# Kernel tuning notes

Measured on AMD Instinct MI355X. Metric: run time of the kernel, lower is better.

Reference implementation:

```python
import jax, jax.numpy as jnp
import numpy as np

B, S, D, E, K = 4, 4096, 2048, 64, 8

def setup_inputs() -> dict:
    key = jax.random.key(0)
    k1, k2 = jax.random.split(key, 2)
    x = jax.random.normal(k1, (B, S, D), dtype=jnp.float32)
    # centroid projection params (Dense(features=n_experts))
    W = jax.random.normal(k2, (D, E), dtype=jnp.float32) / np.sqrt(D).astype(np.float32)
    b = jnp.zeros((E,), dtype=jnp.float32)
    return {"x": x, "W": W, "b": b, "k": K}

def reference(x, W, b, k):
    # dense gating projection + sigmoid -> per-token expert scores [B,S,E]
    scores = jax.nn.sigmoid(jnp.einsum('bsd,de->bse', x, W) + b)
    # per-token top-k expert selection (vectorized form of apply_along_axis(top))
    g_i, idx = jax.lax.top_k(scores, k)          # [B,S,k]
    g = g_i / jnp.sum(g_i, axis=-1, keepdims=True)  # renormalize top-k gates
    return g, idx, scores
```

## Files before the change

### kernel.cpp

```cpp
#include <hip/hip_runtime.h>
#include <math.h>
#include <stdint.h>

#define NTOK   16384
#define DDIM   2048
#define NE     64
#define TOPK   8

#define THREADS 512
#define TOKPB   32
#define BK      64
#define NCHUNK  (DDIM / BK)

#define XSLOTS   (TOKPB * (BK / 4))
#define WSLOTS   (BK * (NE / 4))
#define BUFSLOTS (XSLOTS + WSLOTS)
#define NBUF     3

__device__ __forceinline__ void gl_lds16(const void* g, void* l) {
    __builtin_amdgcn_global_load_lds(
        (const __attribute__((address_space(1))) void*)(uintptr_t)g,
        (__attribute__((address_space(3))) void*)(uintptr_t)l,
        16, 0, 0);
}

__global__ __launch_bounds__(THREADS, 4) void gate_kernel(
    const float* __restrict__ x, const float* __restrict__ W,
    const float* __restrict__ b, float* __restrict__ out)
{
    __shared__ float4 smem[NBUF * BUFSLOTS];

    const int tid  = threadIdx.x;
    const int wave = tid >> 6;
    const int ks   = tid >> 5;
    const int p    = tid & 31;
    const int tg   = p >> 3;
    const int eg   = p & 7;
    const int tok0 = blockIdx.x * TOKPB;

    const int st_t  = tid >> 4;
    const int st_kp = tid & 15;
    const float* gx  = x + (size_t)(tok0 + st_t) * DDIM
                         + 4 * (st_kp ^ ((st_t >> 3) & 3));
    const float* gw0 = W + (size_t)st_t        * NE + 4 * (st_kp ^ wave);
    const float* gw1 = W + (size_t)(st_t + 32) * NE + 4 * (st_kp ^ wave);

    auto stage = [&](int c) {
        float4* Bf = &smem[(c % NBUF) * BUFSLOTS];
        const int kc = c * BK;
        gl_lds16(gx + kc,               &Bf[wave * 64]);
        gl_lds16(gw0 + (size_t)kc * NE, &Bf[XSLOTS + wave * 64]);
        gl_lds16(gw1 + (size_t)kc * NE, &Bf[XSLOTS + 512 + wave * 64]);
    };

    float acc[8][8];
#pragma unroll
    for (int i = 0; i < 8; ++i)
#pragma unroll
        for (int j = 0; j < 8; ++j) acc[i][j] = 0.f;

    auto compute = [&](int c) {
        const float4* BX = &smem[(c % NBUF) * BUFSLOTS];
        const float4* BW = BX + XSLOTS;
        float4 wreg[4][2];
#pragma unroll
        for (int kk = 0; kk < 4; ++kk) {
            const int k = ks * 4 + kk;
            wreg[kk][0] = BW[k * 16 + ((eg * 2)     ^ (ks & 7))];
            wreg[kk][1] = BW[k * 16 + ((eg * 2 + 1) ^ (ks & 7))];
        }
#pragma unroll
        for (int i = 0; i < 8; ++i) {
            const float4 xv = BX[(tg * 8 + i) * 16 + (ks ^ tg)];
            const float* xp = (const float*)&xv;
#pragma unroll
            for (int kk = 0; kk < 4; ++kk) {
                const float xs = xp[kk];
                const float* w0 = (const float*)&wreg[kk][0];
                const float* w1 = (const float*)&wreg[kk][1];
#pragma unroll
                for (int m = 0; m < 4; ++m) {
                    acc[i][m]     = fmaf(xs, w0[m], acc[i][m]);
                    acc[i][4 + m] = fmaf(xs, w1[m], acc[i][4 + m]);
                }
            }
        }
    };

    stage(0); stage(1);
#pragma unroll 1
    for (int c = 0; c < NCHUNK - 1; ++c) {
        asm volatile("s_waitcnt vmcnt(3)" ::: "memory");
        __builtin_amdgcn_s_barrier();
        if (c + 2 < NCHUNK) stage(c + 2);
        compute(c);
    }
    asm volatile("s_waitcnt vmcnt(0)" ::: "memory");
    __builtin_amdgcn_s_barrier();
    compute(NCHUNK - 1);
    __syncthreads();

#pragma unroll
    for (int i = 0; i < 8; ++i)
#pragma unroll
        for (int j = 0; j < 8; ++j)
            acc[i][j] += __shfl_xor(acc[i][j], 32);

    float* part = (float*)smem;
    if ((tid & 63) < 32) {
        float* dst = part + wave * 2176 + p * 68;
#pragma unroll
        for (int fq = 0; fq < 16; ++fq) {
            const int i = fq >> 1, h = fq & 1;
            *(float4*)(dst + fq * 4) = make_float4(
                acc[i][h * 4], acc[i][h * 4 + 1],
                acc[i][h * 4 + 2], acc[i][h * 4 + 3]);
        }
    }
    __syncthreads();

    const int t  = tid >> 4;
    const int e4 = tid & 15;
    const int cp = ((t >> 3) << 3) + (e4 >> 1);
    const int cf = ((t & 7) << 1) + (e4 & 1);
    const float4* pf4 = (const float4*)part;
    float sx = 0.f, sy = 0.f, sz = 0.f, sw = 0.f;
#pragma unroll
    for (int w = 0; w < 8; ++w) {
        const float4 v = pf4[w * 544 + cp * 17 + cf];
        sx += v.x; sy += v.y; sz += v.z; sw += v.w;
    }
    __syncthreads();

    const float4 bv = *(const float4*)(b + e4 * 4);
    float4 sg;
    sg.x = 1.f / (1.f + expf(-(sx + bv.x)));
    sg.y = 1.f / (1.f + expf(-(sy + bv.y)));
    sg.z = 1.f / (1.f + expf(-(sz + bv.z)));
    sg.w = 1.f / (1.f + expf(-(sw + bv.w)));

    float* out_g   = out;
    float* out_idx = out + (size_t)NTOK * TOPK;
    float* out_s   = out + (size_t)NTOK * TOPK * 2;

    *(float4*)(out_s + (size_t)(tok0 + t) * NE + e4 * 4) = sg;
    float4* sc4 = (float4*)part;
    sc4[t * 17 + e4] = sg;
    __syncthreads();

    if (tid < 256) {
        const int tt = tid >> 3, lg = tid & 7;
        const float4 a0 = sc4[tt * 17 + lg * 2];
        const float4 a1 = sc4[tt * 17 + lg * 2 + 1];
        float s[8] = {a0.x, a0.y, a0.z, a0.w, a1.x, a1.y, a1.z, a1.w};
        float vsel = 0.f; int esel = 0; float ssum = 0.f;
#pragma unroll
        for (int j = 0; j < TOPK; ++j) {
            float bvv = s[0]; int be = 0;
#pragma unroll
            for (int m = 1; m < 8; ++m)
                if (s[m] > bvv) { bvv = s[m]; be = m; }
            float v = bvv; int ec = lg * 8 + be;
#pragma unroll
            for (int d = 1; d < 8; d <<= 1) {
                const float ov = __shfl_xor(v, d);
                const int   oe = __shfl_xor(ec, d);
                if (ov > v || (ov == v && oe < ec)) { v = ov; ec = oe; }
            }
            ssum += v;
            if (lg == j) { vsel = v; esel = ec; }
            if ((ec >> 3) == lg) {
                const int sl = ec & 7;
#pragma unroll
                for (int m = 0; m < 8; ++m)
                    if (sl == m) s[m] = -1.f;
            }
        }
        const float inv = 1.f / ssum;
        out_g  [(size_t)(tok0 + tt) * TOPK + lg] = vsel * inv;
        out_idx[(size_t)(tok0 + tt) * TOPK + lg] = (float)esel;
    }
}

extern "C" void kernel_launch(void* const* d_in, const int* in_sizes, int n_in,
                              void* d_out, int out_size, void* d_ws, size_t ws_size,
                              hipStream_t stream) {
    const float* x = (const float*)d_in[0];
    const float* W = (const float*)d_in[1];
    const float* b = (const float*)d_in[2];
    float* out = (float*)d_out;
    gate_kernel<<<NTOK / TOKPB, THREADS, 0, stream>>>(x, W, b, out);
}
```

Measured before the change: 221.9 us.

## Halve tokens per block, double-buffer, and remap threads to raise occupancy

Cuts tokens per block from 32 to 16 and gives each thread 8x4 accumulators instead of 8x8. Replaces the triple-buffered vmcnt pipeline with a double buffer guarded by a full barrier. Removes the LDS XOR swizzles and wraps compute in s_setprio, with launch bounds raised to 6 blocks per CU. The aim is higher occupancy and fewer registers. In exchange, W tiles are loaded twice as often per token, and the pipeline is shallower with more blocking syncs.

```diff
diff --git a/kernel.cpp b/kernel.cpp
--- a/kernel.cpp
+++ b/kernel.cpp
@@ -8,14 +8,14 @@
 #define TOPK   8
 
 #define THREADS 512
-#define TOKPB   32
+#define TOKPB   16
 #define BK      64
 #define NCHUNK  (DDIM / BK)
 
 #define XSLOTS   (TOKPB * (BK / 4))
 #define WSLOTS   (BK * (NE / 4))
 #define BUFSLOTS (XSLOTS + WSLOTS)
-#define NBUF     3
+#define SMEMF4   (2 * BUFSLOTS)
 
 __device__ __forceinline__ void gl_lds16(const void* g, void* l) {
     __builtin_amdgcn_global_load_lds(
@@ -24,131 +24,120 @@
         16, 0, 0);
 }
 
-__global__ __launch_bounds__(THREADS, 4) void gate_kernel(
+__global__ __launch_bounds__(THREADS, 6) void gate_kernel(
     const float* __restrict__ x, const float* __restrict__ W,
     const float* __restrict__ b, float* __restrict__ out)
 {
-    __shared__ float4 smem[NBUF * BUFSLOTS];
+    __shared__ float4 smem[SMEMF4];
 
     const int tid  = threadIdx.x;
     const int wave = tid >> 6;
+    const int lane = tid & 63;
     const int ks   = tid >> 5;
-    const int p    = tid & 31;
-    const int tg   = p >> 3;
-    const int eg   = p & 7;
+    const int tg   = (tid >> 4) & 1;
+    const int eg   = tid & 15;
     const int tok0 = blockIdx.x * TOKPB;
 
-    const int st_t  = tid >> 4;
-    const int st_kp = tid & 15;
-    const float* gx  = x + (size_t)(tok0 + st_t) * DDIM
-                         + 4 * (st_kp ^ ((st_t >> 3) & 3));
-    const float* gw0 = W + (size_t)st_t        * NE + 4 * (st_kp ^ wave);
-    const float* gw1 = W + (size_t)(st_t + 32) * NE + 4 * (st_kp ^ wave);
+    const float* gx  = x + (size_t)(tok0 + wave * 4 + (lane >> 4)) * DDIM
+                         + (lane & 15) * 4;
+    const float* gw0 = W + (size_t)(wave * 8 + (lane >> 4)) * NE + (lane & 15) * 4;
+    const float* gw1 = gw0 + (size_t)4 * NE;
 
     auto stage = [&](int c) {
-        float4* Bf = &smem[(c % NBUF) * BUFSLOTS];
+        float4* Bf = &smem[(c & 1) * BUFSLOTS];
         const int kc = c * BK;
-        gl_lds16(gx + kc,               &Bf[wave * 64]);
-        gl_lds16(gw0 + (size_t)kc * NE, &Bf[XSLOTS + wave * 64]);
-        gl_lds16(gw1 + (size_t)kc * NE, &Bf[XSLOTS + 512 + wave * 64]);
+        if (wave < 4) gl_lds16(gx + kc, &Bf[wave * 64]);
+        gl_lds16(gw0 + (size_t)kc * NE, &Bf[XSLOTS + wave * 128]);
+        gl_lds16(gw1 + (size_t)kc * NE, &Bf[XSLOTS + wave * 128 + 64]);
     };
 
-    float acc[8][8];
+    float acc[8][4];
 #pragma unroll
     for (int i = 0; i < 8; ++i)
 #pragma unroll
-        for (int j = 0; j < 8; ++j) acc[i][j] = 0.f;
+        for (int m = 0; m < 4; ++m) acc[i][m] = 0.f;
 
     auto compute = [&](int c) {
-        const float4* BX = &smem[(c % NBUF) * BUFSLOTS];
+        const float4* BX = &smem[(c & 1) * BUFSLOTS];
         const float4* BW = BX + XSLOTS;
-        float4 wreg[4][2];
+        float4 wreg[4];
 #pragma unroll
-        for (int kk = 0; kk < 4; ++kk) {
-            const int k = ks * 4 + kk;
-            wreg[kk][0] = BW[k * 16 + ((eg * 2)     ^ (ks & 7))];
-            wreg[kk][1] = BW[k * 16 + ((eg * 2 + 1) ^ (ks & 7))];
-        }
+        for (int kk = 0; kk < 4; ++kk)
+            wreg[kk] = BW[(ks * 4 + kk) * 16 + eg];
 #pragma unroll
         for (int i = 0; i < 8; ++i) {
-            const float4 xv = BX[(tg * 8 + i) * 16 + (ks ^ tg)];
+            const float4 xv = BX[(tg * 8 + i) * 16 + ks];
             const float* xp = (const float*)&xv;
 #pragma unroll
             for (int kk = 0; kk < 4; ++kk) {
                 const float xs = xp[kk];
-                const float* w0 = (const float*)&wreg[kk][0];
-                const float* w1 = (const float*)&wreg[kk][1];
+                const float* wp = (const float*)&wreg[kk];
 #pragma unroll
-                for (int m = 0; m < 4; ++m) {
-                    acc[i][m]     = fmaf(xs, w0[m], acc[i][m]);
-                    acc[i][4 + m] = fmaf(xs, w1[m], acc[i][4 + m]);
-                }
+                for (int m = 0; m < 4; ++m)
+                    acc[i][m] = fmaf(xs, wp[m], acc[i][m]);
             }
         }
     };
 
-    stage(0); stage(1);
+    stage(0);
 #pragma unroll 1
-    for (int c = 0; c < NCHUNK - 1; ++c) {
-        asm volatile("s_waitcnt vmcnt(3)" ::: "memory");
-        __builtin_amdgcn_s_barrier();
-        if (c + 2 < NCHUNK) stage(c + 2);
+    for (int c = 0; c < NCHUNK; ++c) {
+        __syncthreads();
+        if (c + 1 < NCHUNK) stage(c + 1);
+        __builtin_amdgcn_s_setprio(1);
         compute(c);
+        __builtin_amdgcn_s_setprio(0);
     }
-    asm volatile("s_waitcnt vmcnt(0)" ::: "memory");
-    __builtin_amdgcn_s_barrier();
-    compute(NCHUNK - 1);
     __syncthreads();
 
 #pragma unroll
     for (int i = 0; i < 8; ++i)
 #pragma unroll
-        for (int j = 0; j < 8; ++j)
-            acc[i][j] += __shfl_xor(acc[i][j], 32);
+        for (int m = 0; m < 4; ++m)
+            acc[i][m] += __shfl_xor(acc[i][m], 32);
 
-    float* part = (float*)smem;
-    if ((tid & 63) < 32) {
-        float* dst = part + wave * 2176 + p * 68;
+    float4* part4 = (float4*)smem;
+    const int p = lane & 31;
+    if (lane < 32) {
+        float4* dst = part4 + (wave * 32 + p) * 9;
 #pragma unroll
-        for (int fq = 0; fq < 16; ++fq) {
-            const int i = fq >> 1, h = fq & 1;
-            *(float4*)(dst + fq * 4) = make_float4(
-                acc[i][h * 4], acc[i][h * 4 + 1],
-                acc[i][h * 4 + 2], acc[i][h * 4 + 3]);
-        }
+        for (int i = 0; i < 8; ++i)
+            dst[i] = make_float4(acc[i][0], acc[i][1], acc[i][2], acc[i][3]);
     }
     __syncthreads();
-
-    const int t  = tid >> 4;
-    const int e4 = tid & 15;
-    const int cp = ((t >> 3) << 3) + (e4 >> 1);
-    const int cf = ((t & 7) << 1) + (e4 & 1);
-    const float4* pf4 = (const float4*)part;
-    float sx = 0.f, sy = 0.f, sz = 0.f, sw = 0.f;
-#pragma unroll
-    for (int w = 0; w < 8; ++w) {
-        const float4 v = pf4[w * 544 + cp * 17 + cf];
-        sx += v.x; sy += v.y; sz += v.z; sw += v.w;
-    }
-    __syncthreads();
-
-    const float4 bv = *(const float4*)(b + e4 * 4);
-    float4 sg;
-    sg.x = 1.f / (1.f + expf(-(sx + bv.x)));
-    sg.y = 1.f / (1.f + expf(-(sy + bv.y)));
-    sg.z = 1.f / (1.f + expf(-(sz + bv.z)));
-    sg.w = 1.f / (1.f + expf(-(sw + bv.w)));
 
     float* out_g   = out;
     float* out_idx = out + (size_t)NTOK * TOPK;
     float* out_s   = out + (size_t)NTOK * TOPK * 2;
 
-    *(float4*)(out_s + (size_t)(tok0 + t) * NE + e4 * 4) = sg;
-    float4* sc4 = (float4*)part;
-    sc4[t * 17 + e4] = sg;
+    const int t  = tid >> 4;
+    const int e4 = tid & 15;
+    float4 sg = make_float4(0.f, 0.f, 0.f, 0.f);
+    if (tid < 256) {
+        const int cp = ((t >> 3) << 4) + e4;
+        const int cf = t & 7;
+        float sx = 0.f, sy = 0.f, sz = 0.f, sw = 0.f;
+#pragma unroll
+        for (int w = 0; w < 8; ++w) {
+            const float4 v = part4[(w * 32 + cp) * 9 + cf];
+            sx += v.x; sy += v.y; sz += v.z; sw += v.w;
+        }
+        const float4 bv = *(const float4*)(b + e4 * 4);
+        sg.x = 1.f / (1.f + expf(-(sx + bv.x)));
+        sg.y = 1.f / (1.f + expf(-(sy + bv.y)));
+        sg.z = 1.f / (1.f + expf(-(sz + bv.z)));
+        sg.w = 1.f / (1.f + expf(-(sw + bv.w)));
+    }
     __syncthreads();
 
+    float4* sc4 = (float4*)smem;
     if (tid < 256) {
+        *(float4*)(out_s + (size_t)(tok0 + t) * NE + e4 * 4) = sg;
+        sc4[t * 17 + e4] = sg;
+    }
+    __syncthreads();
+
+    if (tid < 128) {
         const int tt = tid >> 3, lg = tid & 7;
         const float4 a0 = sc4[tt * 17 + lg * 2];
         const float4 a1 = sc4[tt * 17 + lg * 2 + 1];
```

New measurement: 248.4 us. 12.0% more time.
